# Optimization experiments

Measured on AMD Instinct MI355X. Metric: run time of the kernel, lower is better.

Reference implementation:

```python
import jax, jax.numpy as jnp
import numpy as np


def _t2p(x):
    # [B, N, C] -> [B, C, H, H]
    B, N, C = x.shape
    H = int(round(N ** 0.5))
    return x.transpose(0, 2, 1).reshape(B, C, H, H)


def _p2t(x):
    # [B, C, H, W] -> [B, H*W, C]
    B, C, H, W = x.shape
    return x.reshape(B, C, H * W).transpose(0, 2, 1)


def _ln(x, g, b, eps=1e-5):
    m = jnp.mean(x, axis=-1, keepdims=True)
    v = jnp.var(x, axis=-1, keepdims=True)
    return (x - m) / jnp.sqrt(v + eps) * g + b


def _spectral(x, cw):
    # x: [B, C, H, W]; cw: [h, w//2+1, C, 2]
    y = x.transpose(0, 3, 2, 1).astype(jnp.float32)  # [B, W, H, C]
    a, b = y.shape[1], y.shape[2]
    f = jnp.fft.rfft2(y, axes=(1, 2), norm='ortho')   # [B, a, b//2+1, C]
    w = cw[..., 0] + 1j * cw[..., 1]
    y = jnp.fft.irfft2(f * w, s=(a, b), axes=(1, 2), norm='ortho')
    return y.transpose(0, 3, 2, 1)                    # [B, C, H, W]


def _branch(tok, cw, ln1_g, ln1_b, ln2_g, ln2_b, W1, b1, W2, b2):
    # tok: [B, N, 8]
    raw = tok
    t1 = _ln(_p2t(_t2p(tok)), ln1_g, ln1_b)
    p1 = _spectral(_t2p(t1), cw)
    t2 = _ln(_p2t(p1), ln2_g, ln2_b)
    h = jax.nn.gelu(t2 @ W1 + b1, approximate=False)  # exact GELU like torch default
    return (h @ W2 + b2) + raw


def setup_inputs() -> dict:
    key = jax.random.key(0)
    ks = jax.random.split(key, 16)
    B, N, D, HID = 256, 320, 768, 8
    inp = {
        'x': jax.random.normal(ks[0], (B, N, D), dtype=jnp.float32),
        'Wd': jax.random.normal(ks[1], (D, HID), dtype=jnp.float32) * 0.02,
        'bd': jax.random.normal(ks[2], (HID,), dtype=jnp.float32) * 0.02,
        'cw_x': jax.random.normal(ks[3], (16, 9, HID, 2), dtype=jnp.float32) * 0.02,
        'cw_z': jax.random.normal(ks[4], (8, 5, HID, 2), dtype=jnp.float32) * 0.02,
        'ln1_g': jnp.ones((HID,), dtype=jnp.float32),
        'ln1_b': jnp.zeros((HID,), dtype=jnp.float32),
        'ln2_g': jnp.ones((HID,), dtype=jnp.float32),
        'ln2_b': jnp.zeros((HID,), dtype=jnp.float32),
        'W1': jax.random.normal(ks[5], (HID, 2 * HID), dtype=jnp.float32) * 0.1,
        'b1': jnp.zeros((2 * HID,), dtype=jnp.float32),
        'W2': jax.random.normal(ks[6], (2 * HID, HID), dtype=jnp.float32) * 0.1,
        'b2': jnp.zeros((HID,), dtype=jnp.float32),
        'Wu': jax.random.normal(ks[7], (HID, D), dtype=jnp.float32) * 0.02,
        'bu': jnp.zeros((D,), dtype=jnp.float32),
    }
    return inp


def reference(x, Wd, bd, cw_x, cw_z, ln1_g, ln1_b, ln2_g, ln2_b, W1, b1, W2, b2, Wu, bu):
    h = x @ Wd + bd               # [B, 320, 8] adapter_down
    z = h[:, :64, :]              # 8x8 template tokens
    xx = h[:, 64:, :]             # 16x16 search tokens
    # NOTE: original code reuses norm_x1/norm_x2/mlp_x for both branches.
    xo = _branch(xx, cw_x, ln1_g, ln1_b, ln2_g, ln2_b, W1, b1, W2, b2)
    zo = _branch(z, cw_z, ln1_g, ln1_b, ln2_g, ln2_b, W1, b1, W2, b2)
    cat = jnp.concatenate([zo, xo], axis=1)  # [B, 320, 8]
    return cat @ Wu + bu          # adapter_up -> [B, 320, 768]
```

## Files before the change

### kernel.cpp

```cpp
#include <hip/hip_runtime.h>
#include <math.h>

#define PI_F 3.14159265358979323846f
#define SWZ16(i) ((i) ^ (((i) >> 4) & 15))
#define SWZ8(i)  ((i) ^ (((i) >> 3) & 7))

__global__ __launch_bounds__(256) void build_tables(
    const float* __restrict__ cw_x, const float* __restrict__ cw_z,
    float* __restrict__ KKx, float* __restrict__ KKz)
{
    int tid = blockIdx.x * 256 + threadIdx.x;
    if (tid < 2048) {
        int c = tid & 7;
        int ab = tid >> 3;
        int a = ab >> 4, b = ab & 15;
        float acc = 0.f;
        for (int u = 0; u < 16; ++u) {
            for (int v = 0; v < 9; ++v) {
                float m = (v == 0 || v == 8) ? 1.f : 2.f;
                int ph = (u * a + v * b) & 15;
                float th = (2.f * PI_F / 16.f) * (float)ph;
                float sn, cs;
                sincosf(th, &sn, &cs);
                const float* wp = cw_x + (size_t)((u * 9 + v) * 8 + c) * 2;
                acc += m * (wp[0] * cs - wp[1] * sn);
            }
        }
        KKx[ab * 8 + c] = acc * (1.f / 256.f);
    } else if (tid < 2048 + 512) {
        int e = tid - 2048;
        int c = e & 7;
        int ab = e >> 3;
        int a = ab >> 3, b = ab & 7;
        float acc = 0.f;
        for (int u = 0; u < 8; ++u) {
            for (int v = 0; v < 5; ++v) {
                float m = (v == 0 || v == 4) ? 1.f : 2.f;
                int ph = (u * a + v * b) & 7;
                float th = (2.f * PI_F / 8.f) * (float)ph;
                float sn, cs;
                sincosf(th, &sn, &cs);
                const float* wp = cw_z + (size_t)((u * 5 + v) * 8 + c) * 2;
                acc += m * (wp[0] * cs - wp[1] * sn);
            }
        }
        KKz[ab * 8 + c] = acc * (1.f / 64.f);
    }
}

__global__ __launch_bounds__(256) void down_proj(
    const float* __restrict__ x, const float* __restrict__ Wd,
    const float* __restrict__ bd, float* __restrict__ h)
{
    __shared__ float4 wds[1536];
    int t = threadIdx.x;
    const float4* Wd4 = (const float4*)Wd;
    #pragma unroll
    for (int j = 0; j < 6; ++j) {
        int i = t + 256 * j;
        wds[SWZ8(i)] = Wd4[i];
    }
    __syncthreads();

    int g = t >> 4;
    int l = t & 15;
    int row0 = blockIdx.x * 64 + g * 4;

    const float4* xr = (const float4*)x + (size_t)row0 * 192;
    float acc[4][8];
    #pragma unroll
    for (int r = 0; r < 4; ++r)
        #pragma unroll
        for (int c = 0; c < 8; ++c) acc[r][c] = 0.f;

    #pragma unroll
    for (int j = 0; j < 12; ++j) {
        float4 v[4];
        #pragma unroll
        for (int r = 0; r < 4; ++r) v[r] = xr[(size_t)r * 192 + l + 16 * j];
        #pragma unroll
        for (int e = 0; e < 4; ++e) {
            int f4 = ((l + 16 * j) * 4 + e) * 2;
            int sw = SWZ8(f4);
            float4 w0 = wds[sw];
            float4 w1 = wds[sw ^ 1];
            #pragma unroll
            for (int r = 0; r < 4; ++r) {
                float xv = (e == 0) ? v[r].x : (e == 1) ? v[r].y : (e == 2) ? v[r].z : v[r].w;
                acc[r][0] += xv * w0.x;  acc[r][1] += xv * w0.y;
                acc[r][2] += xv * w0.z;  acc[r][3] += xv * w0.w;
                acc[r][4] += xv * w1.x;  acc[r][5] += xv * w1.y;
                acc[r][6] += xv * w1.z;  acc[r][7] += xv * w1.w;
            }
        }
    }
    #pragma unroll
    for (int off = 1; off < 16; off <<= 1)
        #pragma unroll
        for (int r = 0; r < 4; ++r)
            #pragma unroll
            for (int c = 0; c < 8; ++c)
                acc[r][c] += __shfl_xor(acc[r][c], off, 64);

    if (l < 4) {
        float o[8];
        #pragma unroll
        for (int c = 0; c < 8; ++c)
            o[c] = (l == 0) ? acc[0][c] : (l == 1) ? acc[1][c] : (l == 2) ? acc[2][c] : acc[3][c];
        float4 b0 = ((const float4*)bd)[0], b1 = ((const float4*)bd)[1];
        float4* hp = (float4*)h + (size_t)(row0 + l) * 2;
        hp[0] = make_float4(o[0] + b0.x, o[1] + b0.y, o[2] + b0.z, o[3] + b0.w);
        hp[1] = make_float4(o[4] + b1.x, o[5] + b1.y, o[6] + b1.z, o[7] + b1.w);
    }
}

__global__ __launch_bounds__(256) void branch_kernel(
    const float* __restrict__ h,
    const float* __restrict__ KKx, const float* __restrict__ KKz,
    const float* __restrict__ g1v, const float* __restrict__ b1v,
    const float* __restrict__ g2v, const float* __restrict__ b2v,
    const float* __restrict__ W1, const float* __restrict__ b1m,
    const float* __restrict__ W2, const float* __restrict__ b2m,
    float* __restrict__ cat)
{
    __shared__ float4 t1s[512];
    __shared__ float4 kks[512];
    __shared__ float sW1[128], sW2[128], sB1[16], sB2[8];
    __shared__ float sG1[8], sH1[8], sG2[8], sH2[8];

    int t = threadIdx.x;
    int bid = blockIdx.x;
    bool isX = (bid >= 64);

    if (t < 128) { sW1[t] = W1[t]; sW2[t] = W2[t]; }
    if (t < 16)  sB1[t] = b1m[t];
    if (t < 8) { sB2[t] = b2m[t]; sG1[t] = g1v[t]; sH1[t] = b1v[t]; sG2[t] = g2v[t]; sH2[t] = b2v[t]; }

    int rowidx;
    if (isX) {
        rowidx = (bid - 64) * 320 + 64 + t;
    } else {
        int w = t >> 6, tz = t & 63;
        rowidx = (bid * 4 + w) * 320 + tz;
    }
    const float4* hp = (const float4*)h + (size_t)rowidx * 2;
    float4 r0 = hp[0], r1 = hp[1];

    if (isX) {
        const float4* K4 = (const float4*)KKx;
        kks[t] = K4[t];  kks[t + 256] = K4[t + 256];
    } else {
        if (t < 128) kks[t] = ((const float4*)KKz)[t];
    }
    __syncthreads();

    float raw[8] = {r0.x, r0.y, r0.z, r0.w, r1.x, r1.y, r1.z, r1.w};
    float mean = 0.f;
    #pragma unroll
    for (int c = 0; c < 8; ++c) mean += raw[c];
    mean *= 0.125f;
    float var = 0.f;
    #pragma unroll
    for (int c = 0; c < 8; ++c) { float d = raw[c] - mean; var += d * d; }
    var *= 0.125f;
    float inv = rsqrtf(var + 1e-5f);
    float t1[8];
    #pragma unroll
    for (int c = 0; c < 8; ++c) t1[c] = (raw[c] - mean) * inv * sG1[c] + sH1[c];

    int base, i0;
    if (isX) { base = 0; i0 = 2 * t; }
    else     { int w = t >> 6, tz = t & 63; base = w * 128; i0 = 2 * tz; }
    t1s[base + SWZ16(i0)]     = make_float4(t1[0], t1[1], t1[2], t1[3]);
    t1s[base + SWZ16(i0 + 1)] = make_float4(t1[4], t1[5], t1[6], t1[7]);
    __syncthreads();

    float s0=0.f,s1=0.f,s2=0.f,s3=0.f,s4=0.f,s5=0.f,s6=0.f,s7=0.f;
    if (isX) {
        int p = t >> 4, q = t & 15;
        for (int da = 0; da < 16; ++da) {
            int qp = (q - da) & 15;
            #pragma unroll
            for (int db = 0; db < 16; ++db) {
                int pp = (p - db) & 15;
                int si = (pp * 16 + qp) * 2;
                int sw = SWZ16(si);
                float4 v0 = t1s[sw];
                float4 v1 = t1s[sw ^ 1];
                int kb = (da * 16 + db) * 2;
                float4 k0 = kks[kb], k1 = kks[kb + 1];
                s0 += k0.x * v0.x;  s1 += k0.y * v0.y;
                s2 += k0.z * v0.z;  s3 += k0.w * v0.w;
                s4 += k1.x * v1.x;  s5 += k1.y * v1.y;
                s6 += k1.z * v1.z;  s7 += k1.w * v1.w;
            }
        }
    } else {
        int w = t >> 6, tz = t & 63;
        int p = tz >> 3, q = tz & 7;
        int tb = w * 128;
        for (int da = 0; da < 8; ++da) {
            int qp = (q - da) & 7;
            #pragma unroll
            for (int db = 0; db < 8; ++db) {
                int pp = (p - db) & 7;
                int si = (pp * 8 + qp) * 2;
                int sw = SWZ16(si);
                float4 v0 = t1s[tb + sw];
                float4 v1 = t1s[tb + (sw ^ 1)];
                int kb = (da * 8 + db) * 2;
                float4 k0 = kks[kb], k1 = kks[kb + 1];
                s0 += k0.x * v0.x;  s1 += k0.y * v0.y;
                s2 += k0.z * v0.z;  s3 += k0.w * v0.w;
                s4 += k1.x * v1.x;  s5 += k1.y * v1.y;
                s6 += k1.z * v1.z;  s7 += k1.w * v1.w;
            }
        }
    }

    float sarr[8] = {s0, s1, s2, s3, s4, s5, s6, s7};
    float m2 = 0.f;
    #pragma unroll
    for (int c = 0; c < 8; ++c) m2 += sarr[c];
    m2 *= 0.125f;
    float v2 = 0.f;
    #pragma unroll
    for (int c = 0; c < 8; ++c) { float d = sarr[c] - m2; v2 += d * d; }
    v2 *= 0.125f;
    float inv2 = rsqrtf(v2 + 1e-5f);
    float t2[8];
    #pragma unroll
    for (int c = 0; c < 8; ++c) t2[c] = (sarr[c] - m2) * inv2 * sG2[c] + sH2[c];

    float hm[16];
    #pragma unroll
    for (int j = 0; j < 16; ++j) {
        float acc = sB1[j];
        #pragma unroll
        for (int c = 0; c < 8; ++c) acc += t2[c] * sW1[c * 16 + j];
        hm[j] = 0.5f * acc * (1.f + erff(acc * 0.70710678118654752f));
    }
    float o[8];
    #pragma unroll
    for (int c = 0; c < 8; ++c) {
        float acc = sB2[c];
        #pragma unroll
        for (int j = 0; j < 16; ++j) acc += hm[j] * sW2[j * 8 + c];
        o[c] = acc + raw[c];
    }
    float4* cp = (float4*)cat + (size_t)rowidx * 2;
    cp[0] = make_float4(o[0], o[1], o[2], o[3]);
    cp[1] = make_float4(o[4], o[5], o[6], o[7]);
}

__global__ __launch_bounds__(192) void up_proj(
    const float* __restrict__ cat, const float* __restrict__ Wu,
    const float* __restrict__ bu, float* __restrict__ out)
{
    __shared__ float crow[128];
    int t = threadIdx.x;
    int row0 = blockIdx.x * 16;
    if (t < 128) crow[t] = cat[(size_t)row0 * 8 + t];
    __syncthreads();

    const float4* Wu4 = (const float4*)Wu;
    float4 wr[8];
    #pragma unroll
    for (int c = 0; c < 8; ++c) wr[c] = Wu4[c * 192 + t];
    float4 bv = ((const float4*)bu)[t];

    float4* outp = (float4*)out + (size_t)row0 * 192 + t;
    #pragma unroll
    for (int r = 0; r < 16; ++r) {
        const float* cr = &crow[r * 8];
        float4 acc = bv;
        #pragma unroll
        for (int c = 0; c < 8; ++c) {
            float cv = cr[c];
            acc.x += cv * wr[c].x;  acc.y += cv * wr[c].y;
            acc.z += cv * wr[c].z;  acc.w += cv * wr[c].w;
        }
        outp[(size_t)r * 192] = acc;
    }
}

extern "C" void kernel_launch(void* const* d_in, const int* in_sizes, int n_in,
                              void* d_out, int out_size, void* d_ws, size_t ws_size,
                              hipStream_t stream)
{
    (void)in_sizes; (void)n_in; (void)out_size; (void)ws_size;
    const float* x    = (const float*)d_in[0];
    const float* Wd   = (const float*)d_in[1];
    const float* bd   = (const float*)d_in[2];
    const float* cw_x = (const float*)d_in[3];
    const float* cw_z = (const float*)d_in[4];
    const float* g1   = (const float*)d_in[5];
    const float* h1   = (const float*)d_in[6];
    const float* g2   = (const float*)d_in[7];
    const float* h2   = (const float*)d_in[8];
    const float* W1   = (const float*)d_in[9];
    const float* b1   = (const float*)d_in[10];
    const float* W2   = (const float*)d_in[11];
    const float* b2   = (const float*)d_in[12];
    const float* Wu   = (const float*)d_in[13];
    const float* bu   = (const float*)d_in[14];
    float* out = (float*)d_out;

    float* h   = (float*)d_ws;
    float* cat = h + 655360;
    float* KKx = cat + 655360;
    float* KKz = KKx + 2048;

    hipLaunchKernelGGL(build_tables, dim3(10), dim3(256), 0, stream, cw_x, cw_z, KKx, KKz);
    hipLaunchKernelGGL(down_proj,    dim3(1280), dim3(256), 0, stream, x, Wd, bd, h);
    hipLaunchKernelGGL(branch_kernel, dim3(320), dim3(256), 0, stream,
                       h, KKx, KKz, g1, h1, g2, h2, W1, b1, W2, b2, cat);
    hipLaunchKernelGGL(up_proj,      dim3(5120), dim3(192), 0, stream, cat, Wu, bu, out);
}
```

Measured before the change: 187.0 us.

## Fuse down-projection, spectral branch and up-projection into one per-batch kernel

Merges the down-projection, both spectral branches and the up-projection into a single kernel with one 320-thread block per batch element. The intermediate h and cat tensors stay in shared memory instead of round-tripping through global memory, and two kernel launches are removed. In exchange, the grid shrinks to 256 blocks with high LDS usage, so occupancy and memory-level parallelism for the large input read and output write drop. The streaming phases now run serially within each block.

```diff
diff --git a/kernel.cpp b/kernel.cpp
--- a/kernel.cpp
+++ b/kernel.cpp
@@ -48,113 +48,101 @@
     }
 }
 
-__global__ __launch_bounds__(256) void down_proj(
+__global__ __launch_bounds__(320) void fused_kernel(
     const float* __restrict__ x, const float* __restrict__ Wd,
-    const float* __restrict__ bd, float* __restrict__ h)
-{
-    __shared__ float4 wds[1536];
-    int t = threadIdx.x;
-    const float4* Wd4 = (const float4*)Wd;
-    #pragma unroll
-    for (int j = 0; j < 6; ++j) {
-        int i = t + 256 * j;
-        wds[SWZ8(i)] = Wd4[i];
-    }
-    __syncthreads();
-
-    int g = t >> 4;
-    int l = t & 15;
-    int row0 = blockIdx.x * 64 + g * 4;
-
-    const float4* xr = (const float4*)x + (size_t)row0 * 192;
-    float acc[4][8];
-    #pragma unroll
-    for (int r = 0; r < 4; ++r)
-        #pragma unroll
-        for (int c = 0; c < 8; ++c) acc[r][c] = 0.f;
-
-    #pragma unroll
-    for (int j = 0; j < 12; ++j) {
-        float4 v[4];
-        #pragma unroll
-        for (int r = 0; r < 4; ++r) v[r] = xr[(size_t)r * 192 + l + 16 * j];
-        #pragma unroll
-        for (int e = 0; e < 4; ++e) {
-            int f4 = ((l + 16 * j) * 4 + e) * 2;
-            int sw = SWZ8(f4);
-            float4 w0 = wds[sw];
-            float4 w1 = wds[sw ^ 1];
-            #pragma unroll
-            for (int r = 0; r < 4; ++r) {
-                float xv = (e == 0) ? v[r].x : (e == 1) ? v[r].y : (e == 2) ? v[r].z : v[r].w;
-                acc[r][0] += xv * w0.x;  acc[r][1] += xv * w0.y;
-                acc[r][2] += xv * w0.z;  acc[r][3] += xv * w0.w;
-                acc[r][4] += xv * w1.x;  acc[r][5] += xv * w1.y;
-                acc[r][6] += xv * w1.z;  acc[r][7] += xv * w1.w;
-            }
-        }
-    }
-    #pragma unroll
-    for (int off = 1; off < 16; off <<= 1)
-        #pragma unroll
-        for (int r = 0; r < 4; ++r)
-            #pragma unroll
-            for (int c = 0; c < 8; ++c)
-                acc[r][c] += __shfl_xor(acc[r][c], off, 64);
-
-    if (l < 4) {
-        float o[8];
-        #pragma unroll
-        for (int c = 0; c < 8; ++c)
-            o[c] = (l == 0) ? acc[0][c] : (l == 1) ? acc[1][c] : (l == 2) ? acc[2][c] : acc[3][c];
-        float4 b0 = ((const float4*)bd)[0], b1 = ((const float4*)bd)[1];
-        float4* hp = (float4*)h + (size_t)(row0 + l) * 2;
-        hp[0] = make_float4(o[0] + b0.x, o[1] + b0.y, o[2] + b0.z, o[3] + b0.w);
-        hp[1] = make_float4(o[4] + b1.x, o[5] + b1.y, o[6] + b1.z, o[7] + b1.w);
-    }
-}
-
-__global__ __launch_bounds__(256) void branch_kernel(
-    const float* __restrict__ h,
+    const float* __restrict__ bd,
     const float* __restrict__ KKx, const float* __restrict__ KKz,
     const float* __restrict__ g1v, const float* __restrict__ b1v,
     const float* __restrict__ g2v, const float* __restrict__ b2v,
     const float* __restrict__ W1, const float* __restrict__ b1m,
     const float* __restrict__ W2, const float* __restrict__ b2m,
-    float* __restrict__ cat)
+    const float* __restrict__ Wu, const float* __restrict__ bu,
+    float* __restrict__ out)
 {
-    __shared__ float4 t1s[512];
-    __shared__ float4 kks[512];
-    __shared__ float sW1[128], sW2[128], sB1[16], sB2[8];
-    __shared__ float sG1[8], sH1[8], sG2[8], sH2[8];
+    __shared__ float4 wds[1536];
+    __shared__ float  hSf[320 * 9];
+    __shared__ float4 kkx[512];
+    __shared__ float4 kkz[128];
+    __shared__ float4 t1x[512];
+    __shared__ float4 t1z[128];
+    __shared__ float  catS[320 * 9];
+    __shared__ float  sW1[128], sW2[128], sB1[16], sB2[8];
+    __shared__ float  sG1[8], sH1[8], sG2[8], sH2[8];
 
     int t = threadIdx.x;
     int bid = blockIdx.x;
-    bool isX = (bid >= 64);
-
+
+    const float4* Wd4 = (const float4*)Wd;
+    for (int i = t; i < 1536; i += 320) wds[SWZ8(i)] = Wd4[i];
+    for (int i = t; i < 512; i += 320) kkx[i] = ((const float4*)KKx)[i];
+    if (t < 128) kkz[t] = ((const float4*)KKz)[t];
     if (t < 128) { sW1[t] = W1[t]; sW2[t] = W2[t]; }
     if (t < 16)  sB1[t] = b1m[t];
     if (t < 8) { sB2[t] = b2m[t]; sG1[t] = g1v[t]; sH1[t] = b1v[t]; sG2[t] = g2v[t]; sH2[t] = b2v[t]; }
-
-    int rowidx;
-    if (isX) {
-        rowidx = (bid - 64) * 320 + 64 + t;
-    } else {
-        int w = t >> 6, tz = t & 63;
-        rowidx = (bid * 4 + w) * 320 + tz;
-    }
-    const float4* hp = (const float4*)h + (size_t)rowidx * 2;
-    float4 r0 = hp[0], r1 = hp[1];
-
-    if (isX) {
-        const float4* K4 = (const float4*)KKx;
-        kks[t] = K4[t];  kks[t + 256] = K4[t + 256];
-    } else {
-        if (t < 128) kks[t] = ((const float4*)KKz)[t];
-    }
+    float bdv[8];
+    #pragma unroll
+    for (int c = 0; c < 8; ++c) bdv[c] = bd[c];
     __syncthreads();
 
-    float raw[8] = {r0.x, r0.y, r0.z, r0.w, r1.x, r1.y, r1.z, r1.w};
+    {
+        int g = t >> 4;
+        int l = t & 15;
+        const float4* x4 = (const float4*)x;
+        for (int p = 0; p < 4; ++p) {
+            int lr0 = g * 16 + p * 4;
+            const float4* xr = x4 + ((size_t)bid * 320 + lr0) * 192;
+            float acc[4][8];
+            #pragma unroll
+            for (int r = 0; r < 4; ++r)
+                #pragma unroll
+                for (int c = 0; c < 8; ++c) acc[r][c] = 0.f;
+            #pragma unroll
+            for (int j = 0; j < 12; ++j) {
+                float4 v[4];
+                #pragma unroll
+                for (int r = 0; r < 4; ++r) v[r] = xr[(size_t)r * 192 + l + 16 * j];
+                #pragma unroll
+                for (int e = 0; e < 4; ++e) {
+                    int f4i = ((l + 16 * j) * 4 + e) * 2;
+                    int sw = SWZ8(f4i);
+                    float4 w0 = wds[sw];
+                    float4 w1 = wds[sw ^ 1];
+                    #pragma unroll
+                    for (int r = 0; r < 4; ++r) {
+                        float xv = (e == 0) ? v[r].x : (e == 1) ? v[r].y : (e == 2) ? v[r].z : v[r].w;
+                        acc[r][0] += xv * w0.x;  acc[r][1] += xv * w0.y;
+                        acc[r][2] += xv * w0.z;  acc[r][3] += xv * w0.w;
+                        acc[r][4] += xv * w1.x;  acc[r][5] += xv * w1.y;
+                        acc[r][6] += xv * w1.z;  acc[r][7] += xv * w1.w;
+                    }
+                }
+            }
+            #pragma unroll
+            for (int off = 1; off < 16; off <<= 1)
+                #pragma unroll
+                for (int r = 0; r < 4; ++r)
+                    #pragma unroll
+                    for (int c = 0; c < 8; ++c)
+                        acc[r][c] += __shfl_xor(acc[r][c], off, 64);
+            if (l < 4) {
+                float o[8];
+                #pragma unroll
+                for (int c = 0; c < 8; ++c)
+                    o[c] = (l == 0) ? acc[0][c] : (l == 1) ? acc[1][c] : (l == 2) ? acc[2][c] : acc[3][c];
+                int lr = lr0 + l;
+                #pragma unroll
+                for (int c = 0; c < 8; ++c) hSf[lr * 9 + c] = o[c] + bdv[c];
+            }
+        }
+    }
+    __syncthreads();
+
+    bool isX = (t < 256);
+    int lr = isX ? (64 + t) : (t - 256);
+    float raw[8];
+    #pragma unroll
+    for (int c = 0; c < 8; ++c) raw[c] = hSf[lr * 9 + c];
+
     float mean = 0.f;
     #pragma unroll
     for (int c = 0; c < 8; ++c) mean += raw[c];
@@ -168,11 +156,16 @@
     #pragma unroll
     for (int c = 0; c < 8; ++c) t1[c] = (raw[c] - mean) * inv * sG1[c] + sH1[c];
 
-    int base, i0;
-    if (isX) { base = 0; i0 = 2 * t; }
-    else     { int w = t >> 6, tz = t & 63; base = w * 128; i0 = 2 * tz; }
-    t1s[base + SWZ16(i0)]     = make_float4(t1[0], t1[1], t1[2], t1[3]);
-    t1s[base + SWZ16(i0 + 1)] = make_float4(t1[4], t1[5], t1[6], t1[7]);
+    if (isX) {
+        int i0 = 2 * t;
+        t1x[SWZ16(i0)]     = make_float4(t1[0], t1[1], t1[2], t1[3]);
+        t1x[SWZ16(i0 + 1)] = make_float4(t1[4], t1[5], t1[6], t1[7]);
+    } else {
+        int tz = t - 256;
+        int i0 = 2 * tz;
+        t1z[SWZ16(i0)]     = make_float4(t1[0], t1[1], t1[2], t1[3]);
+        t1z[SWZ16(i0 + 1)] = make_float4(t1[4], t1[5], t1[6], t1[7]);
+    }
     __syncthreads();
 
     float s0=0.f,s1=0.f,s2=0.f,s3=0.f,s4=0.f,s5=0.f,s6=0.f,s7=0.f;
@@ -185,10 +178,10 @@
                 int pp = (p - db) & 15;
                 int si = (pp * 16 + qp) * 2;
                 int sw = SWZ16(si);
-                float4 v0 = t1s[sw];
-                float4 v1 = t1s[sw ^ 1];
+                float4 v0 = t1x[sw];
+                float4 v1 = t1x[sw ^ 1];
                 int kb = (da * 16 + db) * 2;
-                float4 k0 = kks[kb], k1 = kks[kb + 1];
+                float4 k0 = kkx[kb], k1 = kkx[kb + 1];
                 s0 += k0.x * v0.x;  s1 += k0.y * v0.y;
                 s2 += k0.z * v0.z;  s3 += k0.w * v0.w;
                 s4 += k1.x * v1.x;  s5 += k1.y * v1.y;
@@ -196,9 +189,8 @@
             }
         }
     } else {
-        int w = t >> 6, tz = t & 63;
+        int tz = t - 256;
         int p = tz >> 3, q = tz & 7;
-        int tb = w * 128;
         for (int da = 0; da < 8; ++da) {
             int qp = (q - da) & 7;
             #pragma unroll
@@ -206,10 +198,10 @@
                 int pp = (p - db) & 7;
                 int si = (pp * 8 + qp) * 2;
                 int sw = SWZ16(si);
-                float4 v0 = t1s[tb + sw];
-                float4 v1 = t1s[tb + (sw ^ 1)];
+                float4 v0 = t1z[sw];
+                float4 v1 = t1z[sw ^ 1];
                 int kb = (da * 8 + db) * 2;
-                float4 k0 = kks[kb], k1 = kks[kb + 1];
+                float4 k0 = kkz[kb], k1 = kkz[kb + 1];
                 s0 += k0.x * v0.x;  s1 += k0.y * v0.y;
                 s2 += k0.z * v0.z;  s3 += k0.w * v0.w;
                 s4 += k1.x * v1.x;  s5 += k1.y * v1.y;
@@ -240,47 +232,48 @@
         for (int c = 0; c < 8; ++c) acc += t2[c] * sW1[c * 16 + j];
         hm[j] = 0.5f * acc * (1.f + erff(acc * 0.70710678118654752f));
     }
-    float o[8];
     #pragma unroll
     for (int c = 0; c < 8; ++c) {
         float acc = sB2[c];
         #pragma unroll
         for (int j = 0; j < 16; ++j) acc += hm[j] * sW2[j * 8 + c];
-        o[c] = acc + raw[c];
-    }
-    float4* cp = (float4*)cat + (size_t)rowidx * 2;
-    cp[0] = make_float4(o[0], o[1], o[2], o[3]);
-    cp[1] = make_float4(o[4], o[5], o[6], o[7]);
-}
-
-__global__ __launch_bounds__(192) void up_proj(
-    const float* __restrict__ cat, const float* __restrict__ Wu,
-    const float* __restrict__ bu, float* __restrict__ out)
-{
-    __shared__ float crow[128];
-    int t = threadIdx.x;
-    int row0 = blockIdx.x * 16;
-    if (t < 128) crow[t] = cat[(size_t)row0 * 8 + t];
+        catS[lr * 9 + c] = acc + raw[c];
+    }
     __syncthreads();
 
-    const float4* Wu4 = (const float4*)Wu;
-    float4 wr[8];
-    #pragma unroll
-    for (int c = 0; c < 8; ++c) wr[c] = Wu4[c * 192 + t];
-    float4 bv = ((const float4*)bu)[t];
-
-    float4* outp = (float4*)out + (size_t)row0 * 192 + t;
-    #pragma unroll
-    for (int r = 0; r < 16; ++r) {
-        const float* cr = &crow[r * 8];
-        float4 acc = bv;
+    {
+        int wv = t >> 6;
+        int ln = t & 63;
+        const float4* Wu4 = (const float4*)Wu;
+        float4 wr[24];
         #pragma unroll
-        for (int c = 0; c < 8; ++c) {
-            float cv = cr[c];
-            acc.x += cv * wr[c].x;  acc.y += cv * wr[c].y;
-            acc.z += cv * wr[c].z;  acc.w += cv * wr[c].w;
-        }
-        outp[(size_t)r * 192] = acc;
+        for (int c = 0; c < 8; ++c)
+            #pragma unroll
+            for (int k = 0; k < 3; ++k)
+                wr[c * 3 + k] = Wu4[c * 192 + ln + 64 * k];
+        float4 bv[3];
+        #pragma unroll
+        for (int k = 0; k < 3; ++k) bv[k] = ((const float4*)bu)[ln + 64 * k];
+
+        for (int r = 0; r < 64; ++r) {
+            int lrow = wv * 64 + r;
+            float cv[8];
+            #pragma unroll
+            for (int c = 0; c < 8; ++c) cv[c] = catS[lrow * 9 + c];
+            float4* o4 = (float4*)out + ((size_t)bid * 320 + lrow) * 192 + ln;
+            #pragma unroll
+            for (int k = 0; k < 3; ++k) {
+                float4 a = bv[k];
+                #pragma unroll
+                for (int c = 0; c < 8; ++c) {
+                    a.x += cv[c] * wr[c * 3 + k].x;
+                    a.y += cv[c] * wr[c * 3 + k].y;
+                    a.z += cv[c] * wr[c * 3 + k].z;
+                    a.w += cv[c] * wr[c * 3 + k].w;
+                }
+                o4[64 * k] = a;
+            }
+        }
     }
 }
 
@@ -306,14 +299,11 @@
     const float* bu   = (const float*)d_in[14];
     float* out = (float*)d_out;
 
-    float* h   = (float*)d_ws;
-    float* cat = h + 655360;
-    float* KKx = cat + 655360;
+    float* KKx = (float*)d_ws;
     float* KKz = KKx + 2048;
 
     hipLaunchKernelGGL(build_tables, dim3(10), dim3(256), 0, stream, cw_x, cw_z, KKx, KKz);
-    hipLaunchKernelGGL(down_proj,    dim3(1280), dim3(256), 0, stream, x, Wd, bd, h);
-    hipLaunchKernelGGL(branch_kernel, dim3(320), dim3(256), 0, stream,
-                       h, KKx, KKz, g1, h1, g2, h2, W1, b1, W2, b2, cat);
-    hipLaunchKernelGGL(up_proj,      dim3(5120), dim3(192), 0, stream, cat, Wu, bu, out);
+    hipLaunchKernelGGL(fused_kernel, dim3(256), dim3(320), 0, stream,
+                       x, Wd, bd, KKx, KKz, g1, h1, g2, h2,
+                       W1, b1, W2, b2, Wu, bu, out);
 }
```

Result: slower. 259.8 us (+39.0%).
